# Performance work log

Measured on AMD Instinct MI355X. Metric: run time of the kernel, lower is better.

Reference implementation:

```python
import jax, jax.numpy as jnp
import numpy as np

DIM = 128
NUM_HEADS = 8


def setup_inputs() -> dict:
    key = jax.random.key(0)
    ks = jax.random.split(key, 5)
    B, L, C = 4, 16384, DIM
    x = jax.random.normal(ks[0], (B, L, C), dtype=jnp.float32)
    # Linear params (stored as (in, out) so y = x @ W + b)
    w_qkv = jax.random.normal(ks[1], (C, 3 * C), dtype=jnp.float32) * (C ** -0.5)
    b_qkv = jax.random.normal(ks[2], (3 * C,), dtype=jnp.float32) * 0.02
    w_proj = jax.random.normal(ks[3], (C, C), dtype=jnp.float32) * (C ** -0.5)
    b_proj = jax.random.normal(ks[4], (C,), dtype=jnp.float32) * 0.02
    return {"x": x, "w_qkv": w_qkv, "b_qkv": b_qkv, "w_proj": w_proj, "b_proj": b_proj}


def reference(x, w_qkv, b_qkv, w_proj, b_proj):
    B, L, C = x.shape
    H = NUM_HEADS
    hd = C // H
    scale = C ** -0.5  # note: torch code scales by dim**-0.5, not head_dim**-0.5

    qkv = x @ w_qkv + b_qkv                      # (B, L, 3C)
    q, k, v = jnp.split(qkv, 3, axis=-1)         # each (B, L, C)

    def to_heads(t):
        return t.reshape(B, L, H, hd).transpose(0, 2, 1, 3)  # (B, H, L, hd)

    q, k, v = to_heads(q), to_heads(k), to_heads(v)

    # Per-token outer product over head_dim: (B, H, L, hd, hd)
    attn = (q * scale)[..., :, None] * k[..., None, :]
    attn = jax.nn.softmax(attn, axis=-1)

    # attn @ v per token: (B, H, L, hd)
    out = jnp.einsum("bhlij,bhlj->bhli", attn, v)
    out = out.transpose(0, 2, 1, 3).reshape(B, L, C)  # (B, L, C)
    return out @ w_proj + b_proj
```

## Files before the change

### kernel.cpp

```cpp
#include <hip/hip_runtime.h>


typedef __attribute__((ext_vector_type(8))) short bf16x8;
typedef __attribute__((ext_vector_type(4))) float f32x4;
typedef __attribute__((ext_vector_type(4))) unsigned int u32x4;

#define TILE_M 32
#define QKV_STRIDE 392
#define PTILE 64
#define O_STRIDE 136

__device__ __forceinline__ unsigned short f2bf(float f) {
    unsigned int u = __builtin_bit_cast(unsigned int, f);
    u += 0x8000u;
    return (unsigned short)(u >> 16);
}
__device__ __forceinline__ unsigned int pkbf(float lo, float hi) {
    unsigned int a = __builtin_bit_cast(unsigned int, lo) + 0x8000u;
    unsigned int b = __builtin_bit_cast(unsigned int, hi) + 0x8000u;
    return __builtin_amdgcn_perm(b, a, 0x07060302u);
}
__device__ __forceinline__ float bflo(unsigned int u) {
    return __builtin_bit_cast(float, u << 16);
}
__device__ __forceinline__ float bfhi(unsigned int u) {
    return __builtin_bit_cast(float, u & 0xffff0000u);
}

__global__ void prep_weights(const float* __restrict__ wqkv,
                             const float* __restrict__ wproj,
                             unsigned short* __restrict__ wqkvT,
                             unsigned short* __restrict__ wprojT) {
    int idx = blockIdx.x * 256 + threadIdx.x;
    if (idx < 384 * 128) {
        int n = idx >> 7, k = idx & 127;
        wqkvT[idx] = f2bf(wqkv[k * 384 + n]);
    }
    if (idx < 128 * 128) {
        int n = idx >> 7, k = idx & 127;
        wprojT[idx] = f2bf(wproj[k * 128 + n]);
    }
}

__global__ __launch_bounds__(256, 4) void qkv_attn(
    const float* __restrict__ x,
    const unsigned short* __restrict__ wqkvT,
    const float* __restrict__ bqkv,
    char* __restrict__ obuf)
{
    __shared__ __align__(16) unsigned short us[TILE_M * QKV_STRIDE];

    const int tid  = threadIdx.x;
    const int lane = tid & 63;
    const int wave = tid >> 6;
    const int col  = lane & 15;
    const int quad = lane >> 4;
    const long base_tok = (long)blockIdx.x * TILE_M;

    const int nb = wave * 6;

    bf16x8 afr[2][4];
#pragma unroll
    for (int m = 0; m < 2; ++m) {
        const float* xrow = x + (base_tok + m * 16 + col) * 128;
        float4 s[4][2];
#pragma unroll
        for (int ks = 0; ks < 4; ++ks) {
            const float4* p = (const float4*)(xrow + ks * 32 + quad * 8);
            s[ks][0] = p[0];
            s[ks][1] = p[1];
        }
#pragma unroll
        for (int ks = 0; ks < 4; ++ks) {
            float4 f0 = s[ks][0], f1 = s[ks][1];
            u32x4 a = {pkbf(f0.x, f0.y), pkbf(f0.z, f0.w),
                       pkbf(f1.x, f1.y), pkbf(f1.z, f1.w)};
            afr[m][ks] = __builtin_bit_cast(bf16x8, a);
        }
    }

    f32x4 acc[2][6];
#pragma unroll
    for (int j = 0; j < 6; ++j) {
        float b = bqkv[(nb + j) * 16 + col];
        acc[0][j] = (f32x4){b, b, b, b};
        acc[1][j] = (f32x4){b, b, b, b};
    }
#pragma unroll
    for (int ks = 0; ks < 4; ++ks) {
        bf16x8 bfr[6];
#pragma unroll
        for (int j = 0; j < 6; ++j)
            bfr[j] = *(const bf16x8*)&wqkvT[((nb + j) * 16 + col) * 128 + ks * 32 + quad * 8];
#pragma unroll
        for (int j = 0; j < 6; ++j) {
            acc[0][j] = __builtin_amdgcn_mfma_f32_16x16x32_bf16(afr[0][ks], bfr[j], acc[0][j], 0, 0, 0);
            acc[1][j] = __builtin_amdgcn_mfma_f32_16x16x32_bf16(afr[1][ks], bfr[j], acc[1][j], 0, 0, 0);
        }
    }

#pragma unroll
    for (int m = 0; m < 2; ++m)
#pragma unroll
        for (int j = 0; j < 6; ++j)
#pragma unroll
            for (int r = 0; r < 4; ++r)
                us[(m * 16 + quad * 4 + r) * QKV_STRIDE + (nb + j) * 16 + col] = f2bf(acc[m][j][r]);
    __syncthreads();

    const int t = tid >> 3;
    const int h = tid & 7;
    const unsigned short* row = us + t * QKV_STRIDE + h * 16;

    u32x4 qp0 = *(const u32x4*)(row);
    u32x4 qp1 = *(const u32x4*)(row + 8);
    u32x4 kp0 = *(const u32x4*)(row + 128);
    u32x4 kp1 = *(const u32x4*)(row + 136);
    u32x4 vp0 = *(const u32x4*)(row + 256);
    u32x4 vp1 = *(const u32x4*)(row + 264);

    const float sl2e = 0.08838834764831845f * 1.44269504088896340f;
    float qv[16], kf[16], vf[16];
#pragma unroll
    for (int c = 0; c < 4; ++c) {
        qv[2*c]   = bflo(qp0[c]); qv[2*c+1]   = bfhi(qp0[c]);
        qv[8+2*c] = bflo(qp1[c]); qv[8+2*c+1] = bfhi(qp1[c]);
        kf[2*c]   = bflo(kp0[c]); kf[2*c+1]   = bfhi(kp0[c]);
        kf[8+2*c] = bflo(kp1[c]); kf[8+2*c+1] = bfhi(kp1[c]);
        vf[2*c]   = bflo(vp0[c]); vf[2*c+1]   = bfhi(vp0[c]);
        vf[8+2*c] = bflo(vp1[c]); vf[8+2*c+1] = bfhi(vp1[c]);
    }
    float ov[16];
#pragma unroll
    for (int i = 0; i < 16; ++i) {
        float qs = qv[i] * sl2e;
        float den = 0.f, num = 0.f;
#pragma unroll
        for (int j = 0; j < 16; ++j) {
            float e = __builtin_amdgcn_exp2f(qs * kf[j]);
            den += e;
            num = fmaf(e, vf[j], num);
        }
        ov[i] = num * __builtin_amdgcn_rcpf(den);
    }
    u32x4 o0 = {pkbf(ov[0], ov[1]), pkbf(ov[2], ov[3]), pkbf(ov[4], ov[5]), pkbf(ov[6], ov[7])};
    u32x4 o1 = {pkbf(ov[8], ov[9]), pkbf(ov[10], ov[11]), pkbf(ov[12], ov[13]), pkbf(ov[14], ov[15])};
    char* orow = obuf + (size_t)(base_tok + t) * 512 + h * 32;
    *(u32x4*)(orow)      = o0;
    *(u32x4*)(orow + 16) = o1;
}

__global__ __launch_bounds__(256) void proj_gemm(
    const char* __restrict__ obuf,
    const unsigned short* __restrict__ wprojT,
    const float* __restrict__ bproj,
    float* __restrict__ out)
{
    __shared__ __align__(16) unsigned short os[PTILE * O_STRIDE];

    const int tid  = threadIdx.x;
    const int lane = tid & 63;
    const int wave = tid >> 6;
    const int col  = lane & 15;
    const int quad = lane >> 4;
    const long base = (long)blockIdx.x * PTILE;

#pragma unroll
    for (int i = 0; i < 4; ++i) {
        int q = tid + 256 * i;
        int r = q >> 4, c = q & 15;
        u32x4 v = *(const u32x4*)(obuf + (size_t)(base + r) * 512 + c * 16);
        *(u32x4*)&os[r * O_STRIDE + c * 8] = v;
    }
    __syncthreads();

    bf16x8 af[4];
#pragma unroll
    for (int ks = 0; ks < 4; ++ks)
        af[ks] = *(const bf16x8*)&os[(wave * 16 + col) * O_STRIDE + ks * 32 + quad * 8];

    f32x4 acc[8];
#pragma unroll
    for (int n = 0; n < 8; ++n) {
        float b = bproj[n * 16 + col];
        acc[n] = (f32x4){b, b, b, b};
    }
#pragma unroll
    for (int ks = 0; ks < 4; ++ks) {
#pragma unroll
        for (int half = 0; half < 2; ++half) {
            bf16x8 bb[4];
#pragma unroll
            for (int n = 0; n < 4; ++n)
                bb[n] = *(const bf16x8*)&wprojT[((half * 4 + n) * 16 + col) * 128 + ks * 32 + quad * 8];
#pragma unroll
            for (int n = 0; n < 4; ++n)
                acc[half * 4 + n] = __builtin_amdgcn_mfma_f32_16x16x32_bf16(
                    af[ks], bb[n], acc[half * 4 + n], 0, 0, 0);
        }
    }
#pragma unroll
    for (int n = 0; n < 8; ++n)
#pragma unroll
        for (int r = 0; r < 4; ++r) {
            long tt = base + wave * 16 + quad * 4 + r;
            out[tt * 128 + n * 16 + col] = acc[n][r];
        }
}

extern "C" void kernel_launch(void* const* d_in, const int* in_sizes, int n_in,
                              void* d_out, int out_size, void* d_ws, size_t ws_size,
                              hipStream_t stream) {
    const float* x     = (const float*)d_in[0];
    const float* wqkv  = (const float*)d_in[1];
    const float* bqkv  = (const float*)d_in[2];
    const float* wproj = (const float*)d_in[3];
    const float* bproj = (const float*)d_in[4];
    float* out = (float*)d_out;

    unsigned short* wqkvT  = (unsigned short*)d_ws;
    unsigned short* wprojT = wqkvT + 384 * 128;

    prep_weights<<<192, 256, 0, stream>>>(wqkv, wproj, wqkvT, wprojT);

    const int tokens = in_sizes[0] / 128;
    qkv_attn<<<tokens / TILE_M, 256, 0, stream>>>(
        x, wqkvT, bqkv, (char*)d_out);
    proj_gemm<<<tokens / PTILE, 256, 0, stream>>>(
        (const char*)d_out, wprojT, bproj, out);
}
```

Baseline: 153.0 us.

## Make each wave own 16 tokens end-to-end to drop block barrier

Reorganizes the QKV+attention kernel so each wave computes the full 384-column QKV projection for its own 16 tokens and then runs the per-token softmax on them from a private shared-memory slice. This removes the block-wide __syncthreads between the GEMM and attention phases and lets waves progress independently. The cost is that each wave now holds 24 accumulators and reloads all of wqkvT rather than a quarter of it. Shared memory per block doubles to 64 tokens, and launch bounds drop to 3 blocks per CU, which may reduce occupancy.

```diff
diff --git a/kernel.cpp b/kernel.cpp
--- a/kernel.cpp
+++ b/kernel.cpp
@@ -5,8 +5,8 @@
 typedef __attribute__((ext_vector_type(4))) float f32x4;
 typedef __attribute__((ext_vector_type(4))) unsigned int u32x4;
 
-#define TILE_M 32
 #define QKV_STRIDE 392
+#define WAVE_LDS (16 * QKV_STRIDE)
 #define PTILE 64
 #define O_STRIDE 136
 
@@ -42,112 +42,109 @@
     }
 }
 
-__global__ __launch_bounds__(256, 4) void qkv_attn(
+__global__ __launch_bounds__(256, 3) void qkv_attn(
     const float* __restrict__ x,
     const unsigned short* __restrict__ wqkvT,
     const float* __restrict__ bqkv,
     char* __restrict__ obuf)
 {
-    __shared__ __align__(16) unsigned short us[TILE_M * QKV_STRIDE];
+    __shared__ __align__(16) unsigned short us[4 * WAVE_LDS];
 
     const int tid  = threadIdx.x;
     const int lane = tid & 63;
     const int wave = tid >> 6;
     const int col  = lane & 15;
     const int quad = lane >> 4;
-    const long base_tok = (long)blockIdx.x * TILE_M;
-
-    const int nb = wave * 6;
-
-    bf16x8 afr[2][4];
-#pragma unroll
-    for (int m = 0; m < 2; ++m) {
-        const float* xrow = x + (base_tok + m * 16 + col) * 128;
-        float4 s[4][2];
-#pragma unroll
-        for (int ks = 0; ks < 4; ++ks) {
-            const float4* p = (const float4*)(xrow + ks * 32 + quad * 8);
-            s[ks][0] = p[0];
-            s[ks][1] = p[1];
-        }
-#pragma unroll
-        for (int ks = 0; ks < 4; ++ks) {
-            float4 f0 = s[ks][0], f1 = s[ks][1];
-            u32x4 a = {pkbf(f0.x, f0.y), pkbf(f0.z, f0.w),
-                       pkbf(f1.x, f1.y), pkbf(f1.z, f1.w)};
-            afr[m][ks] = __builtin_bit_cast(bf16x8, a);
-        }
-    }
-
-    f32x4 acc[2][6];
-#pragma unroll
-    for (int j = 0; j < 6; ++j) {
-        float b = bqkv[(nb + j) * 16 + col];
-        acc[0][j] = (f32x4){b, b, b, b};
-        acc[1][j] = (f32x4){b, b, b, b};
-    }
-#pragma unroll
-    for (int ks = 0; ks < 4; ++ks) {
-        bf16x8 bfr[6];
-#pragma unroll
-        for (int j = 0; j < 6; ++j)
-            bfr[j] = *(const bf16x8*)&wqkvT[((nb + j) * 16 + col) * 128 + ks * 32 + quad * 8];
-#pragma unroll
-        for (int j = 0; j < 6; ++j) {
-            acc[0][j] = __builtin_amdgcn_mfma_f32_16x16x32_bf16(afr[0][ks], bfr[j], acc[0][j], 0, 0, 0);
-            acc[1][j] = __builtin_amdgcn_mfma_f32_16x16x32_bf16(afr[1][ks], bfr[j], acc[1][j], 0, 0, 0);
-        }
-    }
-
-#pragma unroll
-    for (int m = 0; m < 2; ++m)
-#pragma unroll
-        for (int j = 0; j < 6; ++j)
-#pragma unroll
-            for (int r = 0; r < 4; ++r)
-                us[(m * 16 + quad * 4 + r) * QKV_STRIDE + (nb + j) * 16 + col] = f2bf(acc[m][j][r]);
-    __syncthreads();
-
-    const int t = tid >> 3;
-    const int h = tid & 7;
-    const unsigned short* row = us + t * QKV_STRIDE + h * 16;
-
-    u32x4 qp0 = *(const u32x4*)(row);
-    u32x4 qp1 = *(const u32x4*)(row + 8);
-    u32x4 kp0 = *(const u32x4*)(row + 128);
-    u32x4 kp1 = *(const u32x4*)(row + 136);
-    u32x4 vp0 = *(const u32x4*)(row + 256);
-    u32x4 vp1 = *(const u32x4*)(row + 264);
+    const long wbase = (long)blockIdx.x * 64 + wave * 16;
+    unsigned short* uw = us + wave * WAVE_LDS;
+
+    const float* xrow = x + (wbase + col) * 128;
+    float4 s[4][2];
+#pragma unroll
+    for (int ks = 0; ks < 4; ++ks) {
+        const float4* p = (const float4*)(xrow + ks * 32 + quad * 8);
+        s[ks][0] = p[0];
+        s[ks][1] = p[1];
+    }
+    bf16x8 afr[4];
+#pragma unroll
+    for (int ks = 0; ks < 4; ++ks) {
+        float4 f0 = s[ks][0], f1 = s[ks][1];
+        u32x4 a = {pkbf(f0.x, f0.y), pkbf(f0.z, f0.w),
+                   pkbf(f1.x, f1.y), pkbf(f1.z, f1.w)};
+        afr[ks] = __builtin_bit_cast(bf16x8, a);
+    }
+
+    f32x4 acc[24];
+#pragma unroll
+    for (int n = 0; n < 24; ++n) {
+        float b = bqkv[n * 16 + col];
+        acc[n] = (f32x4){b, b, b, b};
+    }
+#pragma unroll
+    for (int ks = 0; ks < 4; ++ks) {
+#pragma unroll
+        for (int g = 0; g < 4; ++g) {
+            bf16x8 bfr[6];
+#pragma unroll
+            for (int j = 0; j < 6; ++j)
+                bfr[j] = *(const bf16x8*)&wqkvT[((g * 6 + j) * 16 + col) * 128 + ks * 32 + quad * 8];
+#pragma unroll
+            for (int j = 0; j < 6; ++j)
+                acc[g * 6 + j] = __builtin_amdgcn_mfma_f32_16x16x32_bf16(
+                    afr[ks], bfr[j], acc[g * 6 + j], 0, 0, 0);
+        }
+    }
+
+#pragma unroll
+    for (int n = 0; n < 24; ++n)
+#pragma unroll
+        for (int r = 0; r < 4; ++r)
+            uw[(quad * 4 + r) * QKV_STRIDE + n * 16 + col] = f2bf(acc[n][r]);
 
     const float sl2e = 0.08838834764831845f * 1.44269504088896340f;
-    float qv[16], kf[16], vf[16];
-#pragma unroll
-    for (int c = 0; c < 4; ++c) {
-        qv[2*c]   = bflo(qp0[c]); qv[2*c+1]   = bfhi(qp0[c]);
-        qv[8+2*c] = bflo(qp1[c]); qv[8+2*c+1] = bfhi(qp1[c]);
-        kf[2*c]   = bflo(kp0[c]); kf[2*c+1]   = bfhi(kp0[c]);
-        kf[8+2*c] = bflo(kp1[c]); kf[8+2*c+1] = bfhi(kp1[c]);
-        vf[2*c]   = bflo(vp0[c]); vf[2*c+1]   = bfhi(vp0[c]);
-        vf[8+2*c] = bflo(vp1[c]); vf[8+2*c+1] = bfhi(vp1[c]);
-    }
-    float ov[16];
-#pragma unroll
-    for (int i = 0; i < 16; ++i) {
-        float qs = qv[i] * sl2e;
-        float den = 0.f, num = 0.f;
-#pragma unroll
-        for (int j = 0; j < 16; ++j) {
-            float e = __builtin_amdgcn_exp2f(qs * kf[j]);
-            den += e;
-            num = fmaf(e, vf[j], num);
-        }
-        ov[i] = num * __builtin_amdgcn_rcpf(den);
-    }
-    u32x4 o0 = {pkbf(ov[0], ov[1]), pkbf(ov[2], ov[3]), pkbf(ov[4], ov[5]), pkbf(ov[6], ov[7])};
-    u32x4 o1 = {pkbf(ov[8], ov[9]), pkbf(ov[10], ov[11]), pkbf(ov[12], ov[13]), pkbf(ov[14], ov[15])};
-    char* orow = obuf + (size_t)(base_tok + t) * 512 + h * 32;
-    *(u32x4*)(orow)      = o0;
-    *(u32x4*)(orow + 16) = o1;
+#pragma unroll
+    for (int p = 0; p < 2; ++p) {
+        const int t16 = (lane >> 3) + 8 * p;
+        const int h   = lane & 7;
+        const unsigned short* row = uw + t16 * QKV_STRIDE + h * 16;
+
+        u32x4 qp0 = *(const u32x4*)(row);
+        u32x4 qp1 = *(const u32x4*)(row + 8);
+        u32x4 kp0 = *(const u32x4*)(row + 128);
+        u32x4 kp1 = *(const u32x4*)(row + 136);
+        u32x4 vp0 = *(const u32x4*)(row + 256);
+        u32x4 vp1 = *(const u32x4*)(row + 264);
+
+        float qv[16], kf[16], vf[16];
+#pragma unroll
+        for (int c = 0; c < 4; ++c) {
+            qv[2*c]   = bflo(qp0[c]); qv[2*c+1]   = bfhi(qp0[c]);
+            qv[8+2*c] = bflo(qp1[c]); qv[8+2*c+1] = bfhi(qp1[c]);
+            kf[2*c]   = bflo(kp0[c]); kf[2*c+1]   = bfhi(kp0[c]);
+            kf[8+2*c] = bflo(kp1[c]); kf[8+2*c+1] = bfhi(kp1[c]);
+            vf[2*c]   = bflo(vp0[c]); vf[2*c+1]   = bfhi(vp0[c]);
+            vf[8+2*c] = bflo(vp1[c]); vf[8+2*c+1] = bfhi(vp1[c]);
+        }
+        float ov[16];
+#pragma unroll
+        for (int i = 0; i < 16; ++i) {
+            float qs = qv[i] * sl2e;
+            float den = 0.f, num = 0.f;
+#pragma unroll
+            for (int j = 0; j < 16; ++j) {
+                float e = __builtin_amdgcn_exp2f(qs * kf[j]);
+                den += e;
+                num = fmaf(e, vf[j], num);
+            }
+            ov[i] = num * __builtin_amdgcn_rcpf(den);
+        }
+        u32x4 o0 = {pkbf(ov[0], ov[1]), pkbf(ov[2], ov[3]), pkbf(ov[4], ov[5]), pkbf(ov[6], ov[7])};
+        u32x4 o1 = {pkbf(ov[8], ov[9]), pkbf(ov[10], ov[11]), pkbf(ov[12], ov[13]), pkbf(ov[14], ov[15])};
+        char* orow = obuf + (size_t)(wbase + t16) * 512 + h * 32;
+        *(u32x4*)(orow)      = o0;
+        *(u32x4*)(orow + 16) = o1;
+    }
 }
 
 __global__ __launch_bounds__(256) void proj_gemm(
@@ -224,7 +221,7 @@
     prep_weights<<<192, 256, 0, stream>>>(wqkv, wproj, wqkvT, wprojT);
 
     const int tokens = in_sizes[0] / 128;
-    qkv_attn<<<tokens / TILE_M, 256, 0, stream>>>(
+    qkv_attn<<<tokens / 64, 256, 0, stream>>>(
         x, wqkvT, bqkv, (char*)d_out);
     proj_gemm<<<tokens / PTILE, 256, 0, stream>>>(
         (const char*)d_out, wprojT, bproj, out);
```

After: 167.5 us. +9.5%, slower.
